# Optimization experiments

Hardware: AMD Instinct MI355X
Metric: run time of the kernel (lower is better)

## Reference

```python
import jax, jax.numpy as jnp
import numpy as np

B, T, I, H, O = 64, 1024, 64, 512, 64


def setup_inputs() -> dict:
    key = jax.random.key(0)
    ks = jax.random.split(key, 8)
    s = 1.0 / np.sqrt(H)  # PyTorch nn.RNN / nn.Linear init scale
    u = lambda k, shape: jax.random.uniform(k, shape, jnp.float32, -s, s)
    return {
        "x": jax.random.normal(ks[0], (B, T, I), jnp.float32),
        "h": jnp.zeros((1, B, H), jnp.float32),
        "W_ih": u(ks[1], (H, I)),
        "W_hh": u(ks[2], (H, H)),
        "b_ih": u(ks[3], (H,)),
        "b_hh": u(ks[4], (H,)),
        "W_out": u(ks[5], (O, H)),
        "b_out": u(ks[6], (O,)),
    }


def reference(x, h, W_ih, W_hh, b_ih, b_hh, W_out, b_out):
    # Precompute input projection for all timesteps: [B, T, H]
    xp = jnp.einsum('bti,hi->bth', x, W_ih) + b_ih + b_hh

    def step(h_prev, xp_t):
        # h_t = tanh(x_t W_ih^T + b_ih + h_{t-1} W_hh^T + b_hh)
        h_t = jnp.tanh(xp_t + h_prev @ W_hh.T)
        return h_t, h_t

    h0 = h[0]  # [B, H]
    h_last, hs = jax.lax.scan(step, h0, jnp.swapaxes(xp, 0, 1))  # hs: [T, B, H]
    hs = jnp.swapaxes(hs, 0, 1)  # [B, T, H]
    out = jnp.tanh(jnp.einsum('bth,oh->bto', hs, W_out) + b_out)  # [B, T, O]
    return out, h_last[None]  # h returned as [1, B, H]
```

## Files before the change

### kernel.cpp

```cpp
#include <hip/hip_runtime.h>
#include <cstdint>
#include <cstddef>


#define BB 64
#define TT 1024
#define II 64
#define HH 512
#define OO 64

__device__ __forceinline__ float tanh_fast(float v) {
  float e = exp2f(fabsf(v) * 2.8853900817779268f);
  float r = 1.0f - 2.0f * __builtin_amdgcn_rcpf(e + 1.0f);
  return copysignf(r, v);
}

__device__ __forceinline__ unsigned f2bf(float f) {
  unsigned u = __float_as_uint(f);
  return (u + 0x7fffu + ((u >> 16) & 1u)) >> 16;
}
__device__ __forceinline__ float bf2f(unsigned b) {
  return __uint_as_float(b << 16);
}

__global__ __launch_bounds__(512, 1) void rnn_persist(
    const float* __restrict__ x, const float* __restrict__ h0,
    const float* __restrict__ Wih, const float* __restrict__ Whh,
    const float* __restrict__ bih, const float* __restrict__ bhh,
    const float* __restrict__ Wout, const float* __restrict__ bout,
    float* __restrict__ out, unsigned long long* __restrict__ ring) {
  const int tid = threadIdx.x;
  const int b   = blockIdx.x & 63;
  const int q   = blockIdx.x >> 6;
  const int n   = tid >> 2;
  const int q4  = tid & 3;
  const int row = q * 128 + n;

  __shared__ float h2[2][4][132];
  __shared__ float x2[2][II];

  float wh[128];
#pragma unroll
  for (int j = 0; j < 32; ++j) {
    const float4 v = *(const float4*)(Whh + (size_t)row * HH + q4 * 128 + j * 4);
    wh[4*j+0] = v.x; wh[4*j+1] = v.y; wh[4*j+2] = v.z; wh[4*j+3] = v.w;
  }
  float wi[16];
#pragma unroll
  for (int j = 0; j < 4; ++j) {
    const float4 v = *(const float4*)(Wih + (size_t)row * II + q4 * 16 + j * 4);
    wi[4*j+0] = v.x; wi[4*j+1] = v.y; wi[4*j+2] = v.z; wi[4*j+3] = v.w;
  }
  const float bias_n = bih[row] + bhh[row];

  const int l     = tid & 63;
  const int oc    = l & 15;
  const int o_loc = (tid >> 6) * 4 + (l >> 4);
  float wo[32];
  float bo = 0.0f;
  if (tid < 256) {
    const int o = q * 16 + o_loc;
#pragma unroll
    for (int j = 0; j < 32; ++j) wo[j] = Wout[(size_t)o * HH + oc + 16 * j];
    bo = bout[o];
  }

  const float* xb           = x + (size_t)b * TT * II;
  unsigned long long* ringb = ring + (size_t)b * 2 * 256;
  float* outb               = out + (size_t)b * TT * OO;

  const bool xloader = (tid >= 256 && tid < 272);
  if (xloader) {
    const int j = tid - 256;
    *(float4*)&x2[1][j * 4] = *(const float4*)(xb + j * 4);
  }

  for (int t = 1; t <= TT + 1; ++t) {
    const int hs = (t - 1) & 1;

    float4 xv;
    if (t < TT && xloader) {
      xv = *(const float4*)(xb + (size_t)t * II + (tid - 256) * 4);
    }

    if (t == 1) {
      if (tid < 256) {
        const int e0 = tid * 2;
        const float2 hv = *(const float2*)(h0 + (size_t)b * HH + e0);
        h2[0][tid >> 6][e0 & 127]       = hv.x;
        h2[0][tid >> 6][(e0 & 127) + 1] = hv.y;
      }
    } else if (tid < 192) {
      const int wq = tid >> 6;
      const int w  = wq + (wq >= q);
      const int m  = tid & 63;
      const unsigned tgt = (unsigned)(t - 1);
      const unsigned long long* p = ringb + (size_t)hs * 256 + w * 64 + m;
      unsigned long long v =
          __hip_atomic_load(p, __ATOMIC_RELAXED, __HIP_MEMORY_SCOPE_AGENT);
      while ((unsigned)(v >> 32) != tgt) {
        v = __hip_atomic_load(p, __ATOMIC_RELAXED, __HIP_MEMORY_SCOPE_AGENT);
      }
      const unsigned lo = (unsigned)v & 0xffffu;
      const unsigned hi = ((unsigned)v >> 16) & 0xffffu;
      *(float2*)&h2[hs][w][2 * m] = make_float2(bf2f(lo), bf2f(hi));
    }
    __syncthreads();

    if (t < TT && xloader) {
      *(float4*)&x2[(t + 1) & 1][(tid - 256) * 4] = xv;
    }

    if (t <= TT) {
      const float* hp = &h2[hs][q4][0];
      float a0 = 0.f, a1 = 0.f, a2 = 0.f, a3 = 0.f;
#pragma unroll
      for (int j = 0; j < 128; j += 4) {
        a0 = fmaf(wh[j+0], hp[j+0], a0);
        a1 = fmaf(wh[j+1], hp[j+1], a1);
        a2 = fmaf(wh[j+2], hp[j+2], a2);
        a3 = fmaf(wh[j+3], hp[j+3], a3);
      }
      float ax = 0.f;
      const float* xp = &x2[t & 1][q4 * 16];
#pragma unroll
      for (int j = 0; j < 16; ++j) ax = fmaf(wi[j], xp[j], ax);

      float a = (a0 + a1) + (a2 + a3) + ax;
      a += __shfl_xor(a, 1);
      a += __shfl_xor(a, 2);
      const float hnew = tanh_fast(a + bias_n);
      const float pv   = __shfl_xor(hnew, 4);
      if (q4 == 0) {
        h2[t & 1][q][n] = hnew;
        if ((n & 1) == 0) {
          const unsigned packed = f2bf(hnew) | (f2bf(pv) << 16);
          __hip_atomic_store(
              ringb + (size_t)(t & 1) * 256 + q * 64 + (n >> 1),
              ((unsigned long long)(unsigned)t << 32) | packed,
              __ATOMIC_RELAXED, __HIP_MEMORY_SCOPE_AGENT);
        }
      }
    }

    if (t >= 2 && tid < 256) {
      float s0 = 0.f, s1 = 0.f;
#pragma unroll
      for (int j = 0; j < 32; j += 2) {
        s0 = fmaf(wo[j+0], h2[hs][(j+0) >> 3][oc + 16 * ((j+0) & 7)], s0);
        s1 = fmaf(wo[j+1], h2[hs][(j+1) >> 3][oc + 16 * ((j+1) & 7)], s1);
      }
      float s = s0 + s1;
      s += __shfl_xor(s, 1);
      s += __shfl_xor(s, 2);
      s += __shfl_xor(s, 4);
      s += __shfl_xor(s, 8);
      if (oc == 0) {
        outb[(size_t)(t - 2) * OO + q * 16 + o_loc] = tanh_fast(s + bo);
      }
    }

    if (t == TT + 1 && q == 0 && tid < 256) {
      const int e0 = tid * 2;
      float* hout = out + (size_t)BB * TT * OO + (size_t)b * HH + e0;
      hout[0] = h2[hs][e0 >> 7][e0 & 127];
      hout[1] = h2[hs][e0 >> 7][(e0 & 127) + 1];
    }
  }
}

extern "C" void kernel_launch(void* const* d_in, const int* in_sizes, int n_in,
                              void* d_out, int out_size, void* d_ws, size_t ws_size,
                              hipStream_t stream) {
  (void)in_sizes; (void)n_in; (void)out_size; (void)ws_size;
  const float* x    = (const float*)d_in[0];
  const float* h0   = (const float*)d_in[1];
  const float* Wih  = (const float*)d_in[2];
  const float* Whh  = (const float*)d_in[3];
  const float* bih  = (const float*)d_in[4];
  const float* bhh  = (const float*)d_in[5];
  const float* Wout = (const float*)d_in[6];
  const float* bout = (const float*)d_in[7];
  float* out = (float*)d_out;

  unsigned long long* ring = (unsigned long long*)d_ws;

  hipMemsetAsync(d_ws, 0, (size_t)BB * 2 * 256 * 8, stream);

  rnn_persist<<<dim3(256), dim3(512), 0, stream>>>(
      x, h0, Wih, Whh, bih, bhh, Wout, bout, out, ring);
}
```

Before: 4.303 ms.

## Add fast sc0 polling ring with slow-ring fallback and per-launch epoch tags

Each h-exchange word is now written to two rings: a fast ring that is stored and polled with sc0 cache-policy global loads and stores, and the original agent-scope atomic ring. Readers first poll the fast ring for a bounded number of tries and fall back permanently to the atomic ring if it does not show up. A persistent epoch counter tags the words, so only the slow ring needs clearing and the larger memset can be partly avoided. This aims to cut cross-block handoff latency on the recurrent critical path. The cost is extra stores, a grid-wide epoch handshake at startup, and reliance on sc0 visibility semantics.

```diff
diff --git a/kernel.cpp b/kernel.cpp
--- a/kernel.cpp
+++ b/kernel.cpp
@@ -8,19 +8,29 @@
 #define II 64
 #define HH 512
 #define OO 64
+#define FAST_CAP 12
 
 __device__ __forceinline__ float tanh_fast(float v) {
   float e = exp2f(fabsf(v) * 2.8853900817779268f);
   float r = 1.0f - 2.0f * __builtin_amdgcn_rcpf(e + 1.0f);
   return copysignf(r, v);
 }
-
 __device__ __forceinline__ unsigned f2bf(float f) {
   unsigned u = __float_as_uint(f);
   return (u + 0x7fffu + ((u >> 16) & 1u)) >> 16;
 }
 __device__ __forceinline__ float bf2f(unsigned b) {
   return __uint_as_float(b << 16);
+}
+__device__ __forceinline__ unsigned long long ld_sc0(const unsigned long long* p) {
+  unsigned long long v;
+  asm volatile("global_load_dwordx2 %0, %1, off sc0\n\ts_waitcnt vmcnt(0)"
+               : "=v"(v) : "v"(p) : "memory");
+  return v;
+}
+__device__ __forceinline__ void st_sc0(unsigned long long* p, unsigned long long w) {
+  asm volatile("global_store_dwordx2 %0, %1, off sc0"
+               :: "v"(p), "v"(w) : "memory");
 }
 
 __global__ __launch_bounds__(512, 1) void rnn_persist(
@@ -28,7 +38,10 @@
     const float* __restrict__ Wih, const float* __restrict__ Whh,
     const float* __restrict__ bih, const float* __restrict__ bhh,
     const float* __restrict__ Wout, const float* __restrict__ bout,
-    float* __restrict__ out, unsigned long long* __restrict__ ring) {
+    float* __restrict__ out, unsigned long long* __restrict__ epoch_cell,
+    unsigned* __restrict__ epoch_bcast,
+    unsigned long long* __restrict__ slowring,
+    unsigned long long* __restrict__ fastring) {
   const int tid = threadIdx.x;
   const int b   = blockIdx.x & 63;
   const int q   = blockIdx.x >> 6;
@@ -38,6 +51,7 @@
 
   __shared__ float h2[2][4][132];
   __shared__ float x2[2][II];
+  __shared__ unsigned s_epoch;
 
   float wh[128];
 #pragma unroll
@@ -65,8 +79,31 @@
     bo = bout[o];
   }
 
+  if (tid == 0) {
+    if (blockIdx.x == 0) {
+      unsigned long long old = __hip_atomic_fetch_add(
+          epoch_cell, 1ull, __ATOMIC_RELAXED, __HIP_MEMORY_SCOPE_AGENT);
+      const unsigned e = (unsigned)old & 0xFFFFFu;
+      __hip_atomic_store(epoch_bcast, (e << 1) | 1u,
+                         __ATOMIC_RELAXED, __HIP_MEMORY_SCOPE_AGENT);
+      s_epoch = e;
+    } else {
+      unsigned v;
+      for (;;) {
+        v = __hip_atomic_load(epoch_bcast, __ATOMIC_RELAXED,
+                              __HIP_MEMORY_SCOPE_AGENT);
+        if (v) break;
+        __builtin_amdgcn_s_sleep(4);
+      }
+      s_epoch = v >> 1;
+    }
+  }
+  __syncthreads();
+  const unsigned epoch = s_epoch;
+
   const float* xb           = x + (size_t)b * TT * II;
-  unsigned long long* ringb = ring + (size_t)b * 2 * 256;
+  unsigned long long* slowb = slowring + (size_t)b * 2 * 256;
+  unsigned long long* fastb = fastring + (size_t)b * 2 * 256;
   float* outb               = out + (size_t)b * TT * OO;
 
   const bool xloader = (tid >= 256 && tid < 272);
@@ -74,6 +111,8 @@
     const int j = tid - 256;
     *(float4*)&x2[1][j * 4] = *(const float4*)(xb + j * 4);
   }
+
+  bool fw = true;
 
   for (int t = 1; t <= TT + 1; ++t) {
     const int hs = (t - 1) & 1;
@@ -94,12 +133,22 @@
       const int wq = tid >> 6;
       const int w  = wq + (wq >= q);
       const int m  = tid & 63;
-      const unsigned tgt = (unsigned)(t - 1);
-      const unsigned long long* p = ringb + (size_t)hs * 256 + w * 64 + m;
-      unsigned long long v =
-          __hip_atomic_load(p, __ATOMIC_RELAXED, __HIP_MEMORY_SCOPE_AGENT);
-      while ((unsigned)(v >> 32) != tgt) {
-        v = __hip_atomic_load(p, __ATOMIC_RELAXED, __HIP_MEMORY_SCOPE_AGENT);
+      const unsigned want = (epoch << 11) | (unsigned)(t - 1);
+      const size_t off = (size_t)hs * 256 + (size_t)w * 64 + m;
+      unsigned long long v = 0;
+      bool got = false;
+      if (fw) {
+        for (int k2 = 0; k2 < FAST_CAP; ++k2) {
+          v = ld_sc0(fastb + off);
+          if ((unsigned)(v >> 32) == want) { got = true; break; }
+        }
+        if (!got) fw = false;
+      }
+      if (!got) {
+        do {
+          v = __hip_atomic_load(slowb + off, __ATOMIC_RELAXED,
+                                __HIP_MEMORY_SCOPE_AGENT);
+        } while ((unsigned)(v >> 32) != want);
       }
       const unsigned lo = (unsigned)v & 0xffffu;
       const unsigned hi = ((unsigned)v >> 16) & 0xffffu;
@@ -135,10 +184,13 @@
         h2[t & 1][q][n] = hnew;
         if ((n & 1) == 0) {
           const unsigned packed = f2bf(hnew) | (f2bf(pv) << 16);
-          __hip_atomic_store(
-              ringb + (size_t)(t & 1) * 256 + q * 64 + (n >> 1),
-              ((unsigned long long)(unsigned)t << 32) | packed,
-              __ATOMIC_RELAXED, __HIP_MEMORY_SCOPE_AGENT);
+          const unsigned long long word =
+              ((unsigned long long)((epoch << 11) | (unsigned)t) << 32) |
+              packed;
+          const size_t off = (size_t)(t & 1) * 256 + (size_t)q * 64 + (n >> 1);
+          st_sc0(fastb + off, word);
+          __hip_atomic_store(slowb + off, word,
+                             __ATOMIC_RELAXED, __HIP_MEMORY_SCOPE_AGENT);
         }
       }
     }
@@ -183,10 +235,15 @@
   const float* bout = (const float*)d_in[7];
   float* out = (float*)d_out;
 
-  unsigned long long* ring = (unsigned long long*)d_ws;
-
-  hipMemsetAsync(d_ws, 0, (size_t)BB * 2 * 256 * 8, stream);
+  unsigned char* ws = (unsigned char*)d_ws;
+  unsigned long long* epoch_cell = (unsigned long long*)ws;
+  unsigned* epoch_bcast          = (unsigned*)(ws + 256);
+  unsigned long long* slowring   = (unsigned long long*)(ws + 4096);
+  unsigned long long* fastring   = (unsigned long long*)(ws + 4096 + 262144);
+
+  hipMemsetAsync(ws + 256, 0, 4096 - 256 + 262144, stream);
 
   rnn_persist<<<dim3(256), dim3(512), 0, stream>>>(
-      x, h0, Wih, Whh, bih, bhh, Wout, bout, out, ring);
-}
+      x, h0, Wih, Whh, bih, bhh, Wout, bout, out,
+      epoch_cell, epoch_bcast, slowring, fastring);
+}
```

After: 4.626 ms. 1.08x slower.
